# Kernel tuning notes

Hardware: AMD Instinct MI355X
Metric: run time of the kernel (lower is better)

The kernel has to match this reference:

```python
import jax, jax.numpy as jnp
import numpy as np

N, E = 50000, 800000
IN_C, OUT_C, D_EMB = 64, 64, 64
NEG_SLOPE = 0.2  # GDN GraphLayer default leaky_relu slope


def setup_inputs() -> dict:
    key = jax.random.key(0)
    ks = jax.random.split(key, 9)
    return {
        "x": jax.random.normal(ks[0], (N, IN_C), jnp.float32),
        "edge_index": jax.random.randint(ks[1], (2, E), 0, N, dtype=jnp.int32),
        "embedding": jax.random.normal(ks[2], (N, D_EMB), jnp.float32),
        # learned params of GraphLayer (heads=1, concat)
        "W": jax.random.normal(ks[3], (OUT_C, IN_C), jnp.float32) * (1.0 / np.sqrt(IN_C)),
        "att_i": jax.random.normal(ks[4], (OUT_C,), jnp.float32) * 0.1,
        "att_j": jax.random.normal(ks[5], (OUT_C,), jnp.float32) * 0.1,
        "att_em_i": jax.random.normal(ks[6], (D_EMB,), jnp.float32) * 0.1,
        "att_em_j": jax.random.normal(ks[7], (D_EMB,), jnp.float32) * 0.1,
        "bias": jax.random.normal(ks[8], (OUT_C,), jnp.float32) * 0.01,
    }


def reference(x, edge_index, embedding, W, att_i, att_j, att_em_i, att_em_j, bias):
    n = x.shape[0]
    loops = jnp.arange(n, dtype=edge_index.dtype)
    src = jnp.concatenate([edge_index[0], loops])  # message source j
    dst = jnp.concatenate([edge_index[1], loops])  # message target i

    h = x @ W.T  # [N, OUT_C]
    # per-node attention scores (equivalent to cat(h, emb) . cat(att, att_em))
    s_i = h @ att_i + embedding @ att_em_i  # [N]
    s_j = h @ att_j + embedding @ att_em_j  # [N]

    alpha = s_i[dst] + s_j[src]                         # [E+N] edge logits
    alpha = jax.nn.leaky_relu(alpha, NEG_SLOPE)
    # softmax over incoming edges of each destination node
    amax = jax.ops.segment_max(alpha, dst, num_segments=n)
    ex = jnp.exp(alpha - amax[dst])
    denom = jax.ops.segment_sum(ex, dst, num_segments=n)
    alpha = ex / (denom[dst] + 1e-16)

    msg = h[src] * alpha[:, None]                       # [E+N, OUT_C]
    out = jax.ops.segment_sum(msg, dst, num_segments=n) + bias
    return jax.nn.relu(out)
```

## Files before the change

kernel.cpp:

```cpp
#include <hip/hip_runtime.h>
#include <hip/hip_bf16.h>
#include <math.h>

#define NEG_SLOPE 0.2f

#define XTA(k, r) ((k) * 64 + ((r) ^ ((((k) >> 2) & 7) << 2)))

#define NBUK 256
#define SCAT 512
#define LCAP 28
#define LSTR 29
#define FCAP 5120
#define FPAD 16

__device__ __forceinline__ void gemm_tile(
    float* lds, int t, int tid,
    const float* __restrict__ x, const float* __restrict__ emb,
    const float* __restrict__ W,
    const float* __restrict__ att_i, const float* __restrict__ att_j,
    const float* __restrict__ att_em_i, const float* __restrict__ att_em_j,
    __hip_bfloat16* __restrict__ h, float* __restrict__ s_i,
    float* __restrict__ s_j, int N)
{
    float* XT = lds;
    float* WT = lds + 4096;

    const int rbase = t * 64;
    const int valid = min(64, N - rbase);

    #pragma unroll
    for (int i = 0; i < 4; ++i) {
        int idx = i * 256 + tid;
        int r = idx >> 4, m = idx & 15;
        float4 v = make_float4(0.f, 0.f, 0.f, 0.f);
        if (r < valid)
            v = *reinterpret_cast<const float4*>(x + (size_t)(rbase + r) * 64 + 4 * m);
        int k = 4 * m;
        XT[XTA(k + 0, r)] = v.x;
        XT[XTA(k + 1, r)] = v.y;
        XT[XTA(k + 2, r)] = v.z;
        XT[XTA(k + 3, r)] = v.w;
    }
    #pragma unroll
    for (int i = 0; i < 4; ++i) {
        int idx = i * 256 + tid;
        int c = idx >> 4, m = idx & 15;
        float4 v = *reinterpret_cast<const float4*>(W + idx * 4);
        int k = 4 * m;
        WT[XTA(k + 0, c)] = v.x;
        WT[XTA(k + 1, c)] = v.y;
        WT[XTA(k + 2, c)] = v.z;
        WT[XTA(k + 3, c)] = v.w;
    }
    __syncthreads();

    const int cg_ = tid & 15, rg = tid >> 4;
    const int c0 = cg_ * 4, r0 = rg * 4;
    float acc[4][4];
    #pragma unroll
    for (int a = 0; a < 4; ++a)
        #pragma unroll
        for (int q = 0; q < 4; ++q) acc[a][q] = 0.f;

    #pragma unroll 4
    for (int k = 0; k < 64; ++k) {
        float4 wv = *reinterpret_cast<float4*>(&WT[XTA(k, c0)]);
        float4 xa = *reinterpret_cast<float4*>(&XT[XTA(k, r0)]);
        float xs[4] = {xa.x, xa.y, xa.z, xa.w};
        float ws[4] = {wv.x, wv.y, wv.z, wv.w};
        #pragma unroll
        for (int a = 0; a < 4; ++a)
            #pragma unroll
            for (int q = 0; q < 4; ++q)
                acc[a][q] = fmaf(ws[a], xs[q], acc[a][q]);
    }

    #pragma unroll
    for (int q = 0; q < 4; ++q) {
        int r = r0 + q;
        if (r < valid) {
            union { __hip_bfloat16 p[4]; uint2 u; } pk;
            pk.p[0] = __float2bfloat16(acc[0][q]);
            pk.p[1] = __float2bfloat16(acc[1][q]);
            pk.p[2] = __float2bfloat16(acc[2][q]);
            pk.p[3] = __float2bfloat16(acc[3][q]);
            *reinterpret_cast<uint2*>(h + (size_t)(rbase + r) * 64 + c0) = pk.u;
        }
    }

    float ai[4], aj[4];
    #pragma unroll
    for (int a = 0; a < 4; ++a) { ai[a] = att_i[c0 + a]; aj[a] = att_j[c0 + a]; }

    __syncthreads();
    float* RED_I = lds;
    float* RED_J = lds + 1088;
    float* EMT   = lds + 4096;

    #pragma unroll
    for (int q = 0; q < 4; ++q) {
        int r = r0 + q;
        float pi = acc[0][q]*ai[0] + acc[1][q]*ai[1] + acc[2][q]*ai[2] + acc[3][q]*ai[3];
        float pj = acc[0][q]*aj[0] + acc[1][q]*aj[1] + acc[2][q]*aj[2] + acc[3][q]*aj[3];
        RED_I[r * 17 + cg_] = pi;
        RED_J[r * 17 + cg_] = pj;
    }
    #pragma unroll
    for (int i = 0; i < 4; ++i) {
        int idx = i * 256 + tid;
        int r = idx >> 4, m = idx & 15;
        float4 v = make_float4(0.f, 0.f, 0.f, 0.f);
        if (r < valid)
            v = *reinterpret_cast<const float4*>(emb + (size_t)(rbase + r) * 64 + 4 * m);
        int k = 4 * m;
        EMT[XTA(k + 0, r)] = v.x;
        EMT[XTA(k + 1, r)] = v.y;
        EMT[XTA(k + 2, r)] = v.z;
        EMT[XTA(k + 3, r)] = v.w;
    }
    __syncthreads();

    if (tid < 64 && tid < valid) {
        float ri = 0.f, rj = 0.f;
        #pragma unroll
        for (int j = 0; j < 16; ++j) {
            ri += RED_I[tid * 17 + j];
            rj += RED_J[tid * 17 + j];
        }
        float ei = 0.f, ej = 0.f;
        #pragma unroll 16
        for (int k = 0; k < 64; ++k) {
            float ev = EMT[XTA(k, tid)];
            ei = fmaf(ev, att_em_i[k], ei);
            ej = fmaf(ev, att_em_j[k], ej);
        }
        s_i[rbase + tid] = ri + ei;
        s_j[rbase + tid] = rj + ej;
    }
}

__global__ __launch_bounds__(256) void k_gemm_scatter(
    const float* __restrict__ x, const float* __restrict__ emb,
    const float* __restrict__ W,
    const float* __restrict__ att_i, const float* __restrict__ att_j,
    const float* __restrict__ att_em_i, const float* __restrict__ att_em_j,
    const int* __restrict__ srcA, const int* __restrict__ dstA,
    int* __restrict__ fcur, unsigned* __restrict__ fifo,
    __hip_bfloat16* __restrict__ h, float* __restrict__ s_i,
    float* __restrict__ s_j, int N, int E, int sh)
{
    __shared__ float lds[8192];
    const int tid = threadIdx.x;

    if ((int)blockIdx.x < SCAT) {
        const int b2 = blockIdx.x;
        int*      lcnt  = reinterpret_cast<int*>(lds);
        unsigned* lst   = reinterpret_cast<unsigned*>(lcnt + NBUK);
        int*      lbase = reinterpret_cast<int*>(lst + NBUK * LSTR);
        for (int i = tid; i < NBUK; i += 256) lcnt[i] = 0;
        __syncthreads();

        const int npos = SCAT * 256;
        const int E4 = E >> 2;
        const int4* d4p = reinterpret_cast<const int4*>(dstA);
        const int4* s4p = reinterpret_cast<const int4*>(srcA);
        const unsigned ml = (1u << sh) - 1u;

        #define PUT(dd, ss) do {                                             \
            int _b = (int)((unsigned)(dd) >> sh);                            \
            unsigned _w = ((unsigned)(ss) << 16) | ((unsigned)(dd) & ml);    \
            int _lp = atomicAdd(&lcnt[_b], 1);                               \
            if (_lp < LCAP) lst[_b * LSTR + _lp] = _w;                       \
            else { int _gp = atomicAdd(&fcur[_b * FPAD], 1);                 \
                   if (_gp < FCAP) fifo[(size_t)_b * FCAP + _gp] = _w; }     \
        } while (0)

        for (int p = b2 * 256 + tid; p < E4; p += npos) {
            int4 d4 = d4p[p];
            int4 s4 = s4p[p];
            PUT(d4.x, s4.x);
            PUT(d4.y, s4.y);
            PUT(d4.z, s4.z);
            PUT(d4.w, s4.w);
        }
        for (int e = E4 * 4 + b2 * 256 + tid; e < E; e += npos) {
            int dd = dstA[e], ss = srcA[e];
            PUT(dd, ss);
        }
        #undef PUT
        __syncthreads();

        {
            int cnt = lcnt[tid];
            if (cnt > LCAP) cnt = LCAP;
            int base = 0;
            if (cnt > 0) base = atomicAdd(&fcur[tid * FPAD], cnt);
            lbase[tid] = base;
        }
        __syncthreads();

        const int lane = tid & 63, wid = tid >> 6;
        #pragma unroll
        for (int g = 0; g < 8; ++g) {
            int b = wid * 64 + g * 8 + (lane >> 3);
            int idx = lane & 7;
            int cnt = lcnt[b];
            if (cnt > LCAP) cnt = LCAP;
            int base = lbase[b];
            for (int i = idx; i < cnt; i += 8) {
                int gp = base + i;
                if (gp < FCAP)
                    fifo[(size_t)b * FCAP + gp] = lst[b * LSTR + i];
            }
        }
        return;
    }

    gemm_tile(lds, blockIdx.x - SCAT, tid, x, emb, W, att_i, att_j,
              att_em_i, att_em_j, h, s_i, s_j, N);
}

__global__ __launch_bounds__(256) void k_place(
    const unsigned* __restrict__ fifo, const int* __restrict__ fcur,
    unsigned short* __restrict__ csr, int* __restrict__ cursor,
    int N, int sh)
{
    __shared__ int lcnt[1024];
    const int tid = threadIdx.x;
    const int b = blockIdx.x;
    const int range = 1 << sh;
    const int base = b << sh;

    for (int i = tid; i < range; i += 256) lcnt[i] = 0;
    __syncthreads();

    int cnt = fcur[b * FPAD];
    if (cnt > FCAP) cnt = FCAP;
    const unsigned* f = fifo + (size_t)b * FCAP;
    for (int i = tid; i < cnt; i += 256) {
        unsigned w = f[i];
        int dloc = (int)(w & (unsigned)(range - 1));
        int s = (int)(w >> 16);
        int pos = atomicAdd(&lcnt[dloc], 1);
        if (pos < 64)
            csr[(size_t)(base + dloc) * 64 + pos] = (unsigned short)s;
    }
    __syncthreads();

    for (int i = tid; i < range; i += 256) {
        int node = base + i;
        if (node < N) cursor[node] = lcnt[i];
    }
}

__global__ __launch_bounds__(256) void k_aggregate(
    const __hip_bfloat16* __restrict__ h, const float* __restrict__ s_i,
    const float* __restrict__ s_j, const int* __restrict__ cursor,
    const unsigned short* __restrict__ csr, const float* __restrict__ bias,
    float* __restrict__ out, int N)
{
    __shared__ uint2 tbl[4][64];
    const int tid  = threadIdx.x;
    const int lane = tid & 63;
    const int wid  = tid >> 6;
    const int node = (blockIdx.x * blockDim.x + tid) >> 6;
    if (node >= N) return;

    int deg_e = cursor[node];
    deg_e = (deg_e > 63) ? 63 : deg_e;
    const int degT = deg_e + 1;
    const float si = s_i[node];

    int s = node;
    if (lane < deg_e) s = csr[(size_t)node * 64 + lane];
    float ex = 0.f;
    if (lane < degT) {
        float a = si + s_j[s];
        a = (a > 0.f) ? a : NEG_SLOPE * a;
        ex = __expf(a);
    }
    float l = ex;
    #pragma unroll
    for (int off = 32; off > 0; off >>= 1) l += __shfl_xor(l, off);

    tbl[wid][lane] = make_uint2(__float_as_uint(ex), (unsigned)s);

    const int e8 = lane >> 3;
    const int c8 = lane & 7;
    const uint4* hp4 = reinterpret_cast<const uint4*>(h);
    float a0 = 0.f, a1 = 0.f, a2 = 0.f, a3 = 0.f;
    float a4 = 0.f, a5 = 0.f, a6 = 0.f, a7 = 0.f;

    const int iters = (degT + 7) >> 3;
    #pragma unroll 2
    for (int it = 0; it < iters; ++it) {
        uint2 rec = tbl[wid][8 * it + e8];
        float e = __uint_as_float(rec.x);
        int   t = (int)rec.y;
        uint4 u = hp4[(size_t)t * 8 + c8];
        a0 = fmaf(e, __uint_as_float(u.x << 16), a0);
        a1 = fmaf(e, __uint_as_float(u.x & 0xffff0000u), a1);
        a2 = fmaf(e, __uint_as_float(u.y << 16), a2);
        a3 = fmaf(e, __uint_as_float(u.y & 0xffff0000u), a3);
        a4 = fmaf(e, __uint_as_float(u.z << 16), a4);
        a5 = fmaf(e, __uint_as_float(u.z & 0xffff0000u), a5);
        a6 = fmaf(e, __uint_as_float(u.w << 16), a6);
        a7 = fmaf(e, __uint_as_float(u.w & 0xffff0000u), a7);
    }

    a0 += __shfl_xor(a0, 8); a0 += __shfl_xor(a0, 16); a0 += __shfl_xor(a0, 32);
    a1 += __shfl_xor(a1, 8); a1 += __shfl_xor(a1, 16); a1 += __shfl_xor(a1, 32);
    a2 += __shfl_xor(a2, 8); a2 += __shfl_xor(a2, 16); a2 += __shfl_xor(a2, 32);
    a3 += __shfl_xor(a3, 8); a3 += __shfl_xor(a3, 16); a3 += __shfl_xor(a3, 32);
    a4 += __shfl_xor(a4, 8); a4 += __shfl_xor(a4, 16); a4 += __shfl_xor(a4, 32);
    a5 += __shfl_xor(a5, 8); a5 += __shfl_xor(a5, 16); a5 += __shfl_xor(a5, 32);
    a6 += __shfl_xor(a6, 8); a6 += __shfl_xor(a6, 16); a6 += __shfl_xor(a6, 32);
    a7 += __shfl_xor(a7, 8); a7 += __shfl_xor(a7, 16); a7 += __shfl_xor(a7, 32);

    if (lane < 8) {
        float inv = 1.f / (l + 1e-16f);
        float4 b0 = *reinterpret_cast<const float4*>(bias + 8 * lane);
        float4 b1 = *reinterpret_cast<const float4*>(bias + 8 * lane + 4);
        float4 o0, o1;
        o0.x = fmaxf(a0 * inv + b0.x, 0.f);
        o0.y = fmaxf(a1 * inv + b0.y, 0.f);
        o0.z = fmaxf(a2 * inv + b0.z, 0.f);
        o0.w = fmaxf(a3 * inv + b0.w, 0.f);
        o1.x = fmaxf(a4 * inv + b1.x, 0.f);
        o1.y = fmaxf(a5 * inv + b1.y, 0.f);
        o1.z = fmaxf(a6 * inv + b1.z, 0.f);
        o1.w = fmaxf(a7 * inv + b1.w, 0.f);
        *reinterpret_cast<float4*>(out + (size_t)node * 64 + 8 * lane)     = o0;
        *reinterpret_cast<float4*>(out + (size_t)node * 64 + 8 * lane + 4) = o1;
    }
}

extern "C" void kernel_launch(void* const* d_in, const int* in_sizes, int n_in,
                              void* d_out, int out_size, void* d_ws, size_t ws_size,
                              hipStream_t stream) {
    const float* x        = (const float*)d_in[0];
    const int*   ei       = (const int*)  d_in[1];
    const float* emb      = (const float*)d_in[2];
    const float* W        = (const float*)d_in[3];
    const float* att_i    = (const float*)d_in[4];
    const float* att_j    = (const float*)d_in[5];
    const float* att_em_i = (const float*)d_in[6];
    const float* att_em_j = (const float*)d_in[7];
    const float* bias     = (const float*)d_in[8];
    float* out = (float*)d_out;

    const int N = in_sizes[0] / 64;
    const int E = in_sizes[1] / 2;
    const int* e_src = ei;
    const int* e_dst = ei + E;

    char* ws = (char*)d_ws;
    __hip_bfloat16* h = (__hip_bfloat16*)ws;  ws += (size_t)N * 64 * 2;
    float* s_i     = (float*)ws;  ws += (size_t)N * 4;
    float* s_j     = (float*)ws;  ws += (size_t)N * 4;
    int*   cursor  = (int*)ws;    ws += (size_t)N * 4;
    unsigned short* csr = (unsigned short*)ws;  ws += (size_t)N * 64 * 2;
    unsigned* fifo = (unsigned*)ws;  ws += (size_t)NBUK * FCAP * 4;
    int*   fcur    = (int*)ws;    ws += NBUK * FPAD * 4;

    int sh = 0;
    while (((N - 1) >> sh) >= NBUK) ++sh;
    const int nbuk_eff = ((N - 1) >> sh) + 1;

    const int GB = (N + 63) / 64;

    hipMemsetAsync(fcur, 0, NBUK * FPAD * sizeof(int), stream);
    k_gemm_scatter<<<SCAT + GB, 256, 0, stream>>>(
        x, emb, W, att_i, att_j, att_em_i, att_em_j,
        e_src, e_dst, fcur, fifo, h, s_i, s_j, N, E, sh);
    k_place<<<nbuk_eff, 256, 0, stream>>>(fifo, fcur, csr, cursor, N, sh);
    k_aggregate<<<(N * 64 + 255) / 256, 256, 0, stream>>>(h, s_i, s_j, cursor,
                                                          csr, bias, out, N);
}
```

Baseline: 143.8 us.

## Compute edge attention exponentials in placement kernel and store with source index

Moves the per-edge leaky-relu/exp computation from the aggregation kernel into the CSR placement kernel, storing (exp, src) pairs as 8-byte records instead of 16-bit source indices. This removes the dependent s_j gather from the aggregation critical path and lets the aggregate wave load ready-made records. It also raises the placement block size to 1024 threads. The cost is four times more CSR storage and traffic, and the placement kernel now does random s_j reads itself. Shrinking lcnt to 256 entries assumes range stays at or below 256.

Result: no change. 145.6 us (+1.3%).

```diff
diff --git a/kernel.cpp b/kernel.cpp
--- a/kernel.cpp
+++ b/kernel.cpp
@@ -220,34 +220,44 @@
               att_em_i, att_em_j, h, s_i, s_j, N);
 }
 
-__global__ __launch_bounds__(256) void k_place(
+__global__ __launch_bounds__(1024) void k_place(
     const unsigned* __restrict__ fifo, const int* __restrict__ fcur,
-    unsigned short* __restrict__ csr, int* __restrict__ cursor,
+    const float* __restrict__ s_i, const float* __restrict__ s_j,
+    uint2* __restrict__ csr2, int* __restrict__ cursor,
     int N, int sh)
 {
-    __shared__ int lcnt[1024];
+    __shared__ int   lcnt[256];
+    __shared__ float sbuf[256];
     const int tid = threadIdx.x;
     const int b = blockIdx.x;
     const int range = 1 << sh;
     const int base = b << sh;
 
-    for (int i = tid; i < range; i += 256) lcnt[i] = 0;
+    for (int i = tid; i < range; i += 1024) {
+        lcnt[i] = 0;
+        int node = base + i;
+        sbuf[i] = (node < N) ? s_i[node] : 0.f;
+    }
     __syncthreads();
 
     int cnt = fcur[b * FPAD];
     if (cnt > FCAP) cnt = FCAP;
     const unsigned* f = fifo + (size_t)b * FCAP;
-    for (int i = tid; i < cnt; i += 256) {
+    for (int i = tid; i < cnt; i += 1024) {
         unsigned w = f[i];
         int dloc = (int)(w & (unsigned)(range - 1));
         int s = (int)(w >> 16);
+        float a = sbuf[dloc] + s_j[s];
+        a = (a > 0.f) ? a : NEG_SLOPE * a;
+        float ex = __expf(a);
         int pos = atomicAdd(&lcnt[dloc], 1);
         if (pos < 64)
-            csr[(size_t)(base + dloc) * 64 + pos] = (unsigned short)s;
-    }
-    __syncthreads();
-
-    for (int i = tid; i < range; i += 256) {
+            csr2[(size_t)(base + dloc) * 64 + pos] =
+                make_uint2(__float_as_uint(ex), (unsigned)s);
+    }
+    __syncthreads();
+
+    for (int i = tid; i < range; i += 1024) {
         int node = base + i;
         if (node < N) cursor[node] = lcnt[i];
     }
@@ -256,7 +266,7 @@
 __global__ __launch_bounds__(256) void k_aggregate(
     const __hip_bfloat16* __restrict__ h, const float* __restrict__ s_i,
     const float* __restrict__ s_j, const int* __restrict__ cursor,
-    const unsigned short* __restrict__ csr, const float* __restrict__ bias,
+    const uint2* __restrict__ csr2, const float* __restrict__ bias,
     float* __restrict__ out, int N)
 {
     __shared__ uint2 tbl[4][64];
@@ -268,22 +278,20 @@
 
     int deg_e = cursor[node];
     deg_e = (deg_e > 63) ? 63 : deg_e;
-    const int degT = deg_e + 1;
-    const float si = s_i[node];
-
-    int s = node;
-    if (lane < deg_e) s = csr[(size_t)node * 64 + lane];
-    float ex = 0.f;
-    if (lane < degT) {
-        float a = si + s_j[s];
+
+    uint2 rec = make_uint2(0u, (unsigned)node);
+    if (lane < deg_e) {
+        rec = csr2[(size_t)node * 64 + lane];
+    } else if (lane == deg_e) {
+        float a = s_i[node] + s_j[node];
         a = (a > 0.f) ? a : NEG_SLOPE * a;
-        ex = __expf(a);
-    }
-    float l = ex;
+        rec.x = __float_as_uint(__expf(a));
+    }
+    float l = __uint_as_float(rec.x);
     #pragma unroll
     for (int off = 32; off > 0; off >>= 1) l += __shfl_xor(l, off);
 
-    tbl[wid][lane] = make_uint2(__float_as_uint(ex), (unsigned)s);
+    tbl[wid][lane] = rec;
 
     const int e8 = lane >> 3;
     const int c8 = lane & 7;
@@ -291,12 +299,13 @@
     float a0 = 0.f, a1 = 0.f, a2 = 0.f, a3 = 0.f;
     float a4 = 0.f, a5 = 0.f, a6 = 0.f, a7 = 0.f;
 
+    const int degT = deg_e + 1;
     const int iters = (degT + 7) >> 3;
     #pragma unroll 2
     for (int it = 0; it < iters; ++it) {
-        uint2 rec = tbl[wid][8 * it + e8];
-        float e = __uint_as_float(rec.x);
-        int   t = (int)rec.y;
+        uint2 r2 = tbl[wid][8 * it + e8];
+        float e = __uint_as_float(r2.x);
+        int   t = (int)r2.y;
         uint4 u = hp4[(size_t)t * 8 + c8];
         a0 = fmaf(e, __uint_as_float(u.x << 16), a0);
         a1 = fmaf(e, __uint_as_float(u.x & 0xffff0000u), a1);
@@ -359,7 +368,7 @@
     float* s_i     = (float*)ws;  ws += (size_t)N * 4;
     float* s_j     = (float*)ws;  ws += (size_t)N * 4;
     int*   cursor  = (int*)ws;    ws += (size_t)N * 4;
-    unsigned short* csr = (unsigned short*)ws;  ws += (size_t)N * 64 * 2;
+    uint2* csr2    = (uint2*)ws;  ws += (size_t)N * 64 * 8;
     unsigned* fifo = (unsigned*)ws;  ws += (size_t)NBUK * FCAP * 4;
     int*   fcur    = (int*)ws;    ws += NBUK * FPAD * 4;
 
@@ -373,7 +382,8 @@
     k_gemm_scatter<<<SCAT + GB, 256, 0, stream>>>(
         x, emb, W, att_i, att_j, att_em_i, att_em_j,
         e_src, e_dst, fcur, fifo, h, s_i, s_j, N, E, sh);
-    k_place<<<nbuk_eff, 256, 0, stream>>>(fifo, fcur, csr, cursor, N, sh);
+    k_place<<<nbuk_eff, 1024, 0, stream>>>(fifo, fcur, s_i, s_j, csr2,
+                                           cursor, N, sh);
     k_aggregate<<<(N * 64 + 255) / 256, 256, 0, stream>>>(h, s_i, s_j, cursor,
-                                                          csr, bias, out, N);
-}
+                                                          csr2, bias, out, N);
+}
```

## Fuse CSR placement and aggregation into one kernel with LDS-resident adjacency

Applied to the files above, without the earlier changes.

Merges the bucket-placement kernel and the aggregation kernel into one launch. Each block takes a quarter of a bucket (64 destination nodes), filters the bucket FIFO for its quarter, builds the per-node source lists in shared memory and aggregates from them directly. This removes the global CSR and cursor round trip and one kernel launch. The cost is that every bucket's FIFO is now read four times, and each 16-wave block walks only 64 nodes. It also skips the h gather for zero-weight edges.

Measured after the change: 144.2 us. No clear change (+0.3%).

```diff
diff --git a/kernel.cpp b/kernel.cpp
--- a/kernel.cpp
+++ b/kernel.cpp
@@ -220,118 +220,115 @@
               att_em_i, att_em_j, h, s_i, s_j, N);
 }
 
-__global__ __launch_bounds__(256) void k_place(
+__global__ __launch_bounds__(1024) void k_place_agg(
     const unsigned* __restrict__ fifo, const int* __restrict__ fcur,
-    unsigned short* __restrict__ csr, int* __restrict__ cursor,
-    int N, int sh)
+    const __hip_bfloat16* __restrict__ h, const float* __restrict__ s_i,
+    const float* __restrict__ s_j, const float* __restrict__ bias,
+    float* __restrict__ out, int N, int sh)
 {
-    __shared__ int lcnt[1024];
+    __shared__ unsigned short csr_l[64][64];
+    __shared__ int   lcnt[64];
+    __shared__ uint2 tbl[16][64];
     const int tid = threadIdx.x;
-    const int b = blockIdx.x;
-    const int range = 1 << sh;
-    const int base = b << sh;
-
-    for (int i = tid; i < range; i += 256) lcnt[i] = 0;
+    const int b   = (int)blockIdx.x >> 2;
+    const int q   = (int)blockIdx.x & 3;
+    const int qbase = (b << sh) + q * 64;
+
+    if (tid < 64) lcnt[tid] = 0;
     __syncthreads();
 
     int cnt = fcur[b * FPAD];
     if (cnt > FCAP) cnt = FCAP;
     const unsigned* f = fifo + (size_t)b * FCAP;
-    for (int i = tid; i < cnt; i += 256) {
+    const unsigned mloc = (1u << sh) - 1u;
+    for (int i = tid; i < cnt; i += 1024) {
         unsigned w = f[i];
-        int dloc = (int)(w & (unsigned)(range - 1));
-        int s = (int)(w >> 16);
-        int pos = atomicAdd(&lcnt[dloc], 1);
-        if (pos < 64)
-            csr[(size_t)(base + dloc) * 64 + pos] = (unsigned short)s;
-    }
-    __syncthreads();
-
-    for (int i = tid; i < range; i += 256) {
-        int node = base + i;
-        if (node < N) cursor[node] = lcnt[i];
-    }
-}
-
-__global__ __launch_bounds__(256) void k_aggregate(
-    const __hip_bfloat16* __restrict__ h, const float* __restrict__ s_i,
-    const float* __restrict__ s_j, const int* __restrict__ cursor,
-    const unsigned short* __restrict__ csr, const float* __restrict__ bias,
-    float* __restrict__ out, int N)
-{
-    __shared__ uint2 tbl[4][64];
-    const int tid  = threadIdx.x;
+        unsigned dloc = w & mloc;
+        if ((int)(dloc >> 6) == q) {
+            int pos = atomicAdd(&lcnt[dloc & 63u], 1);
+            if (pos < 64)
+                csr_l[dloc & 63u][pos] = (unsigned short)(w >> 16);
+        }
+    }
+    __syncthreads();
+
     const int lane = tid & 63;
     const int wid  = tid >> 6;
-    const int node = (blockIdx.x * blockDim.x + tid) >> 6;
-    if (node >= N) return;
-
-    int deg_e = cursor[node];
-    deg_e = (deg_e > 63) ? 63 : deg_e;
-    const int degT = deg_e + 1;
-    const float si = s_i[node];
-
-    int s = node;
-    if (lane < deg_e) s = csr[(size_t)node * 64 + lane];
-    float ex = 0.f;
-    if (lane < degT) {
-        float a = si + s_j[s];
-        a = (a > 0.f) ? a : NEG_SLOPE * a;
-        ex = __expf(a);
-    }
-    float l = ex;
-    #pragma unroll
-    for (int off = 32; off > 0; off >>= 1) l += __shfl_xor(l, off);
-
-    tbl[wid][lane] = make_uint2(__float_as_uint(ex), (unsigned)s);
-
-    const int e8 = lane >> 3;
-    const int c8 = lane & 7;
     const uint4* hp4 = reinterpret_cast<const uint4*>(h);
-    float a0 = 0.f, a1 = 0.f, a2 = 0.f, a3 = 0.f;
-    float a4 = 0.f, a5 = 0.f, a6 = 0.f, a7 = 0.f;
-
-    const int iters = (degT + 7) >> 3;
-    #pragma unroll 2
-    for (int it = 0; it < iters; ++it) {
-        uint2 rec = tbl[wid][8 * it + e8];
-        float e = __uint_as_float(rec.x);
-        int   t = (int)rec.y;
-        uint4 u = hp4[(size_t)t * 8 + c8];
-        a0 = fmaf(e, __uint_as_float(u.x << 16), a0);
-        a1 = fmaf(e, __uint_as_float(u.x & 0xffff0000u), a1);
-        a2 = fmaf(e, __uint_as_float(u.y << 16), a2);
-        a3 = fmaf(e, __uint_as_float(u.y & 0xffff0000u), a3);
-        a4 = fmaf(e, __uint_as_float(u.z << 16), a4);
-        a5 = fmaf(e, __uint_as_float(u.z & 0xffff0000u), a5);
-        a6 = fmaf(e, __uint_as_float(u.w << 16), a6);
-        a7 = fmaf(e, __uint_as_float(u.w & 0xffff0000u), a7);
-    }
-
-    a0 += __shfl_xor(a0, 8); a0 += __shfl_xor(a0, 16); a0 += __shfl_xor(a0, 32);
-    a1 += __shfl_xor(a1, 8); a1 += __shfl_xor(a1, 16); a1 += __shfl_xor(a1, 32);
-    a2 += __shfl_xor(a2, 8); a2 += __shfl_xor(a2, 16); a2 += __shfl_xor(a2, 32);
-    a3 += __shfl_xor(a3, 8); a3 += __shfl_xor(a3, 16); a3 += __shfl_xor(a3, 32);
-    a4 += __shfl_xor(a4, 8); a4 += __shfl_xor(a4, 16); a4 += __shfl_xor(a4, 32);
-    a5 += __shfl_xor(a5, 8); a5 += __shfl_xor(a5, 16); a5 += __shfl_xor(a5, 32);
-    a6 += __shfl_xor(a6, 8); a6 += __shfl_xor(a6, 16); a6 += __shfl_xor(a6, 32);
-    a7 += __shfl_xor(a7, 8); a7 += __shfl_xor(a7, 16); a7 += __shfl_xor(a7, 32);
-
-    if (lane < 8) {
-        float inv = 1.f / (l + 1e-16f);
-        float4 b0 = *reinterpret_cast<const float4*>(bias + 8 * lane);
-        float4 b1 = *reinterpret_cast<const float4*>(bias + 8 * lane + 4);
-        float4 o0, o1;
-        o0.x = fmaxf(a0 * inv + b0.x, 0.f);
-        o0.y = fmaxf(a1 * inv + b0.y, 0.f);
-        o0.z = fmaxf(a2 * inv + b0.z, 0.f);
-        o0.w = fmaxf(a3 * inv + b0.w, 0.f);
-        o1.x = fmaxf(a4 * inv + b1.x, 0.f);
-        o1.y = fmaxf(a5 * inv + b1.y, 0.f);
-        o1.z = fmaxf(a6 * inv + b1.z, 0.f);
-        o1.w = fmaxf(a7 * inv + b1.w, 0.f);
-        *reinterpret_cast<float4*>(out + (size_t)node * 64 + 8 * lane)     = o0;
-        *reinterpret_cast<float4*>(out + (size_t)node * 64 + 8 * lane + 4) = o1;
+
+    #pragma unroll 1
+    for (int j = 0; j < 4; ++j) {
+        const int node_local = wid * 4 + j;
+        const int node = qbase + node_local;
+        if (node >= N) break;
+
+        int deg_e = lcnt[node_local];
+        deg_e = (deg_e > 63) ? 63 : deg_e;
+        const int degT = deg_e + 1;
+        const float si = s_i[node];
+
+        int s = node;
+        if (lane < deg_e) s = (int)csr_l[node_local][lane];
+        float ex = 0.f;
+        if (lane < degT) {
+            float a = si + s_j[s];
+            a = (a > 0.f) ? a : NEG_SLOPE * a;
+            ex = __expf(a);
+        }
+        float l = ex;
+        #pragma unroll
+        for (int off = 32; off > 0; off >>= 1) l += __shfl_xor(l, off);
+
+        tbl[wid][lane] = make_uint2(__float_as_uint(ex), (unsigned)s);
+
+        const int e8 = lane >> 3;
+        const int c8 = lane & 7;
+        float a0 = 0.f, a1 = 0.f, a2 = 0.f, a3 = 0.f;
+        float a4 = 0.f, a5 = 0.f, a6 = 0.f, a7 = 0.f;
+
+        const int iters = (degT + 7) >> 3;
+        #pragma unroll 2
+        for (int it = 0; it < iters; ++it) {
+            uint2 r2 = tbl[wid][8 * it + e8];
+            float e = __uint_as_float(r2.x);
+            if (e != 0.f) {
+                uint4 u = hp4[(size_t)r2.y * 8 + c8];
+                a0 = fmaf(e, __uint_as_float(u.x << 16), a0);
+                a1 = fmaf(e, __uint_as_float(u.x & 0xffff0000u), a1);
+                a2 = fmaf(e, __uint_as_float(u.y << 16), a2);
+                a3 = fmaf(e, __uint_as_float(u.y & 0xffff0000u), a3);
+                a4 = fmaf(e, __uint_as_float(u.z << 16), a4);
+                a5 = fmaf(e, __uint_as_float(u.z & 0xffff0000u), a5);
+                a6 = fmaf(e, __uint_as_float(u.w << 16), a6);
+                a7 = fmaf(e, __uint_as_float(u.w & 0xffff0000u), a7);
+            }
+        }
+
+        a0 += __shfl_xor(a0, 8); a0 += __shfl_xor(a0, 16); a0 += __shfl_xor(a0, 32);
+        a1 += __shfl_xor(a1, 8); a1 += __shfl_xor(a1, 16); a1 += __shfl_xor(a1, 32);
+        a2 += __shfl_xor(a2, 8); a2 += __shfl_xor(a2, 16); a2 += __shfl_xor(a2, 32);
+        a3 += __shfl_xor(a3, 8); a3 += __shfl_xor(a3, 16); a3 += __shfl_xor(a3, 32);
+        a4 += __shfl_xor(a4, 8); a4 += __shfl_xor(a4, 16); a4 += __shfl_xor(a4, 32);
+        a5 += __shfl_xor(a5, 8); a5 += __shfl_xor(a5, 16); a5 += __shfl_xor(a5, 32);
+        a6 += __shfl_xor(a6, 8); a6 += __shfl_xor(a6, 16); a6 += __shfl_xor(a6, 32);
+        a7 += __shfl_xor(a7, 8); a7 += __shfl_xor(a7, 16); a7 += __shfl_xor(a7, 32);
+
+        if (lane < 8) {
+            float inv = 1.f / (l + 1e-16f);
+            float4 b0 = *reinterpret_cast<const float4*>(bias + 8 * lane);
+            float4 b1 = *reinterpret_cast<const float4*>(bias + 8 * lane + 4);
+            float4 o0, o1;
+            o0.x = fmaxf(a0 * inv + b0.x, 0.f);
+            o0.y = fmaxf(a1 * inv + b0.y, 0.f);
+            o0.z = fmaxf(a2 * inv + b0.z, 0.f);
+            o0.w = fmaxf(a3 * inv + b0.w, 0.f);
+            o1.x = fmaxf(a4 * inv + b1.x, 0.f);
+            o1.y = fmaxf(a5 * inv + b1.y, 0.f);
+            o1.z = fmaxf(a6 * inv + b1.z, 0.f);
+            o1.w = fmaxf(a7 * inv + b1.w, 0.f);
+            *reinterpret_cast<float4*>(out + (size_t)node * 64 + 8 * lane)     = o0;
+            *reinterpret_cast<float4*>(out + (size_t)node * 64 + 8 * lane + 4) = o1;
+        }
     }
 }
 
@@ -358,8 +355,6 @@
     __hip_bfloat16* h = (__hip_bfloat16*)ws;  ws += (size_t)N * 64 * 2;
     float* s_i     = (float*)ws;  ws += (size_t)N * 4;
     float* s_j     = (float*)ws;  ws += (size_t)N * 4;
-    int*   cursor  = (int*)ws;    ws += (size_t)N * 4;
-    unsigned short* csr = (unsigned short*)ws;  ws += (size_t)N * 64 * 2;
     unsigned* fifo = (unsigned*)ws;  ws += (size_t)NBUK * FCAP * 4;
     int*   fcur    = (int*)ws;    ws += NBUK * FPAD * 4;
 
@@ -373,7 +368,6 @@
     k_gemm_scatter<<<SCAT + GB, 256, 0, stream>>>(
         x, emb, W, att_i, att_j, att_em_i, att_em_j,
         e_src, e_dst, fcur, fifo, h, s_i, s_j, N, E, sh);
-    k_place<<<nbuk_eff, 256, 0, stream>>>(fifo, fcur, csr, cursor, N, sh);
-    k_aggregate<<<(N * 64 + 255) / 256, 256, 0, stream>>>(h, s_i, s_j, cursor,
-                                                          csr, bias, out, N);
+    k_place_agg<<<nbuk_eff * 4, 1024, 0, stream>>>(fifo, fcur, h, s_i, s_j,
+                                                   bias, out, N, sh);
 }
```
